# Kernel tuning notes

Hardware: AMD Instinct MI355X
Metric: run time of the kernel (lower is better)

## Reference

```python
import jax, jax.numpy as jnp
import numpy as np

B, K, DIN, D, NH, HD, FF = 16384, 64, 49, 16, 2, 8, 32
EPS = 1e-5


def _ln(x, g, b):
    m = jnp.mean(x, axis=-1, keepdims=True)
    v = jnp.mean((x - m) ** 2, axis=-1, keepdims=True)
    return (x - m) / jnp.sqrt(v + EPS) * g + b


def setup_inputs() -> dict:
    key = jax.random.key(0)
    ks = jax.random.split(key, 20)
    s = 0.05
    return {
        "x": jax.random.normal(ks[0], (B, K, DIN), dtype=jnp.float32),
        # torch Linear layout: weight is [out, in]
        "proj_w": jax.random.normal(ks[1], (D, DIN), dtype=jnp.float32) * s,
        "proj_b": jax.random.normal(ks[2], (D,), dtype=jnp.float32) * s,
        "pos": jax.random.normal(ks[3], (1, K, D), dtype=jnp.float32) * s,
        "in_proj_w": jax.random.normal(ks[4], (3 * D, D), dtype=jnp.float32) * s,
        "in_proj_b": jax.random.normal(ks[5], (3 * D,), dtype=jnp.float32) * s,
        "out_w": jax.random.normal(ks[6], (D, D), dtype=jnp.float32) * s,
        "out_b": jax.random.normal(ks[7], (D,), dtype=jnp.float32) * s,
        "ln1_g": jnp.ones((D,), dtype=jnp.float32),
        "ln1_b": jnp.zeros((D,), dtype=jnp.float32),
        "lin1_w": jax.random.normal(ks[8], (FF, D), dtype=jnp.float32) * s,
        "lin1_b": jax.random.normal(ks[9], (FF,), dtype=jnp.float32) * s,
        "lin2_w": jax.random.normal(ks[10], (D, FF), dtype=jnp.float32) * s,
        "lin2_b": jax.random.normal(ks[11], (D,), dtype=jnp.float32) * s,
        "ln2_g": jnp.ones((D,), dtype=jnp.float32),
        "ln2_b": jnp.zeros((D,), dtype=jnp.float32),
        "head_w": jax.random.normal(ks[12], (1, D), dtype=jnp.float32) * s,
        "head_b": jax.random.normal(ks[13], (1,), dtype=jnp.float32) * s,
    }


def reference(x, proj_w, proj_b, pos, in_proj_w, in_proj_b, out_w, out_b,
              ln1_g, ln1_b, lin1_w, lin1_b, lin2_w, lin2_b, ln2_g, ln2_b,
              head_w, head_b):
    # input projection + learned positional embedding
    h = jnp.einsum("bki,di->bkd", x, proj_w) + proj_b + pos  # [B,K,D]

    # --- self-attention (torch MultiheadAttention, post-norm encoder layer) ---
    qkv = jnp.einsum("bkd,ed->bke", h, in_proj_w) + in_proj_b  # [B,K,3D]
    q, k, v = jnp.split(qkv, 3, axis=-1)
    q = q.reshape(B, K, NH, HD)
    k = k.reshape(B, K, NH, HD)
    v = v.reshape(B, K, NH, HD)
    scores = jnp.einsum("bqhd,bkhd->bhqk", q, k) / jnp.sqrt(jnp.float32(HD))
    attn = jax.nn.softmax(scores, axis=-1)
    ctx = jnp.einsum("bhqk,bkhd->bqhd", attn, v).reshape(B, K, D)
    attn_out = jnp.einsum("bkd,od->bko", ctx, out_w) + out_b
    h = _ln(h + attn_out, ln1_g, ln1_b)

    # --- FFN (relu), post-norm ---
    ff = jnp.einsum("bkd,fd->bkf", h, lin1_w) + lin1_b
    ff = jax.nn.relu(ff)
    ff = jnp.einsum("bkf,df->bkd", ff, lin2_w) + lin2_b
    h = _ln(h + ff, ln2_g, ln2_b)

    # mean pool over sequence, then scalar head
    pooled = h.mean(axis=1)  # [B,D]
    out = jnp.einsum("bd,od->bo", pooled, head_w) + head_b
    return out.squeeze(-1)  # [B]
```

## Files before the change

### kernel.cpp

```cpp
#include <hip/hip_runtime.h>


#define XR   0
#define XRS  72
#define HR   4608
#define HRS  40
#define KR   7168
#define KRS  40
#define VTB  9728
#define VTS  72
#define RED  10880
#define SMTOT 10888

#define WS_HB   2304
#define WS_EP   3328

typedef __bf16 v8bf __attribute__((ext_vector_type(8)));
typedef float  v4f  __attribute__((ext_vector_type(4)));

#define LDS_ORDER() __asm__ volatile("" ::: "memory")

static __device__ __forceinline__ short f2bs(float f) {
    __bf16 h = (__bf16)f;
    return __builtin_bit_cast(short, h);
}
#define MFMA(a,b,c) __builtin_amdgcn_mfma_f32_16x16x32_bf16((a),(b),(c),0,0,0)

__global__ __launch_bounds__(64)
void tx_prep(const float* __restrict__ proj_w, const float* __restrict__ proj_b,
             const float* __restrict__ pos,
             const float* __restrict__ in_proj_w, const float* __restrict__ in_proj_b,
             const float* __restrict__ out_w, const float* __restrict__ out_b,
             const float* __restrict__ ln1_g, const float* __restrict__ ln1_b,
             const float* __restrict__ lin1_w, const float* __restrict__ lin1_b,
             const float* __restrict__ lin2_w, const float* __restrict__ lin2_b,
             const float* __restrict__ ln2_g, const float* __restrict__ ln2_b,
             const float* __restrict__ head_w, float* __restrict__ ws)
{
    const int lane = threadIdx.x, g = lane >> 4, c = lane & 15;
    v8bf* wf = (v8bf*)ws;
    v8bf F;
    #pragma unroll
    for (int j = 0; j < 8; ++j) F[j] = (__bf16)proj_w[c*49 + g*8 + j];
    wf[0*64 + lane] = F;
    #pragma unroll
    for (int j = 0; j < 8; ++j) { int k = 32 + g*8 + j; F[j] = (k < 49) ? (__bf16)proj_w[c*49 + k] : (__bf16)0.f; }
    wf[1*64 + lane] = F;
    #pragma unroll
    for (int nt = 0; nt < 3; ++nt) {
        #pragma unroll
        for (int j = 0; j < 8; ++j) { int k = g*8 + j; F[j] = (k < 16) ? (__bf16)in_proj_w[(nt*16 + c)*16 + k] : (__bf16)0.f; }
        wf[(2 + nt)*64 + lane] = F;
    }
    #pragma unroll
    for (int j = 0; j < 8; ++j) { int k = g*8 + j; F[j] = (k < 16) ? (__bf16)out_w[c*16 + k] : (__bf16)0.f; }
    wf[5*64 + lane] = F;
    #pragma unroll
    for (int nt = 0; nt < 2; ++nt) {
        #pragma unroll
        for (int j = 0; j < 8; ++j) { int k = g*8 + j; F[j] = (k < 16) ? (__bf16)lin1_w[(nt*16 + c)*16 + k] : (__bf16)0.f; }
        wf[(6 + nt)*64 + lane] = F;
    }
    #pragma unroll
    for (int j = 0; j < 8; ++j) F[j] = (__bf16)lin2_w[c*32 + g*8 + j];
    wf[8*64 + lane] = F;

    float* hb = ws + WS_HB;
    #pragma unroll
    for (int ww = 0; ww < 4; ++ww)
        #pragma unroll
        for (int r = 0; r < 4; ++r)
            hb[ww*256 + r*64 + lane] = proj_b[c] + pos[(ww*16 + g*4 + r)*16 + c];

    if (lane < 16) {
        float* ep = ws + WS_EP + lane*16;
        ep[0]  = in_proj_b[lane];
        ep[1]  = in_proj_b[16 + lane];
        ep[2]  = in_proj_b[32 + lane];
        ep[3]  = out_b[lane];
        ep[4]  = ln1_g[lane];
        ep[5]  = ln1_b[lane];
        ep[6]  = lin1_b[lane];
        ep[7]  = lin1_b[16 + lane];
        ep[8]  = lin2_b[lane];
        ep[9]  = ln2_g[lane];
        ep[10] = ln2_b[lane];
        ep[11] = head_w[lane];
        ep[12] = 0.f; ep[13] = 0.f; ep[14] = 0.f; ep[15] = 0.f;
    }
}

__global__ __launch_bounds__(256, 7)
void tx_main(const float* __restrict__ x, const float* __restrict__ ws,
             const float* __restrict__ head_b, float* __restrict__ out)
{
    __shared__ __align__(16) short sm[SMTOT];
    const int tid   = threadIdx.x;
    const int w     = tid >> 6;
    const int lane  = tid & 63;
    const int g     = lane >> 4;
    const int c     = lane & 15;
    const int b     = blockIdx.x;
    const int myrow = w*16 + c;
    const int tok0  = w*16 + g*4;
    const int sw    = (c >> 2) & 3;
    const v8bf* wf  = (const v8bf*)ws;
    const float4* ep4 = (const float4*)(ws + WS_EP);

    v8bf zfrag;
    #pragma unroll
    for (int j = 0; j < 8; ++j) zfrag[j] = (__bf16)0.f;

    const float4* xb4 = (const float4*)(x + (size_t)b * 3136);
    #pragma unroll
    for (int i = 0; i < 3; ++i) {
        int idx = tid + i*256;
        float4 v = xb4[idx];
        float vv[4] = {v.x, v.y, v.z, v.w};
        int flat = idx*4;
        #pragma unroll
        for (int e = 0; e < 4; ++e) {
            int f = flat + e, row = f / 49, col = f - row*49;
            int cs = (((col >> 3) ^ ((row >> 2) & 3)) << 3) | (col & 7);
            sm[XR + row*XRS + cs] = f2bs(vv[e]);
        }
    }
    if (tid < 16) {
        int idx = 768 + tid;
        float4 v = xb4[idx];
        float vv[4] = {v.x, v.y, v.z, v.w};
        int flat = idx*4;
        #pragma unroll
        for (int e = 0; e < 4; ++e) {
            int f = flat + e, row = f / 49, col = f - row*49;
            int cs = (((col >> 3) ^ ((row >> 2) & 3)) << 3) | (col & 7);
            sm[XR + row*XRS + cs] = f2bs(vv[e]);
        }
    }
    #pragma unroll
    for (int j = 0; j < 4; ++j) {
        int col = 49 + g*4 + j;
        if (col < 64) {
            int cs = (((col >> 3) ^ sw) << 3) | (col & 7);
            sm[XR + myrow*XRS + cs] = 0;
        }
    }
    *(unsigned long long*)&sm[HR + myrow*HRS + 16 + g*4] = 0ull;
    __syncthreads();

    v4f hC;
    {
        v8bf Bp0 = wf[0*64 + lane], Bp1 = wf[1*64 + lane];
        v8bf a0 = *(const v8bf*)&sm[XR + myrow*XRS + ((g ^ sw) << 3)];
        v8bf a1 = *(const v8bf*)&sm[XR + myrow*XRS + 32 + ((g ^ sw) << 3)];
        v4f z = {0.f, 0.f, 0.f, 0.f};
        hC = MFMA(a0, Bp0, z);
        hC = MFMA(a1, Bp1, hC);
        const float* hb = ws + WS_HB;
        #pragma unroll
        for (int r = 0; r < 4; ++r) hC[r] += hb[w*256 + r*64 + lane];
        #pragma unroll
        for (int r = 0; r < 4; ++r) sm[HR + (tok0 + r)*HRS + c] = f2bs(hC[r]);
    }
    LDS_ORDER();

    {
        v8bf Bq0 = wf[2*64 + lane], Bq1 = wf[3*64 + lane], Bq2 = wf[4*64 + lane];
        v8bf a = *(const v8bf*)&sm[HR + myrow*HRS + g*8];
        v4f z = {0.f, 0.f, 0.f, 0.f};
        v4f qC = MFMA(a, Bq0, z);
        v4f kC = MFMA(a, Bq1, z);
        v4f vC = MFMA(a, Bq2, z);
        float4 e0 = ep4[c*4];
        #pragma unroll
        for (int r = 0; r < 4; ++r) {
            int tok = tok0 + r;
            sm[HR + tok*HRS + c]   = f2bs(qC[r] + e0.x);
            sm[KR + tok*KRS + c]   = f2bs(kC[r] + e0.y);
            sm[VTB + c*VTS + tok]  = f2bs(vC[r] + e0.z);
        }
    }
    __syncthreads();

    v4f ctxC0, ctxC1;
    {
        v8bf aq = *(const v8bf*)&sm[HR + myrow*HRS + g*8];
        const float SC = 0.510069729f;
        #pragma unroll
        for (int hh = 0; hh < 2; ++hh) {
            v4f sC[4];
            #pragma unroll
            for (int tj = 0; tj < 4; ++tj) {
                v8bf bk = zfrag;
                if (g == hh) bk = *(const v8bf*)&sm[KR + (tj*16 + c)*KRS + g*8];
                v4f z = {0.f, 0.f, 0.f, 0.f};
                sC[tj] = MFMA(aq, bk, z);
            }
            #pragma unroll
            for (int tj = 0; tj < 4; ++tj) {
                int cl = ((((tj*2) + (c >> 3)) ^ g) << 3) | (c & 7);
                #pragma unroll
                for (int r = 0; r < 4; ++r)
                    sm[XR + (tok0 + r)*XRS + cl] = f2bs(exp2f(sC[tj][r] * SC));
            }
            v8bf bv0 = zfrag, bv1 = zfrag;
            bool act  = (hh == 0) ? (c < 8) : (c >= 8);
            int  onec = (hh == 0) ? 8 : 7;
            if (act) {
                bv0 = *(const v8bf*)&sm[VTB + c*VTS + g*8];
                bv1 = *(const v8bf*)&sm[VTB + c*VTS + 32 + g*8];
            } else if (c == onec) {
                #pragma unroll
                for (int j = 0; j < 8; ++j) { bv0[j] = (__bf16)1.f; bv1[j] = (__bf16)1.f; }
            }
            LDS_ORDER();
            v4f acc = {0.f, 0.f, 0.f, 0.f};
            acc = MFMA(*(const v8bf*)&sm[XR + myrow*XRS + ((g ^ sw) << 3)],      bv0, acc);
            acc = MFMA(*(const v8bf*)&sm[XR + myrow*XRS + 32 + ((g ^ sw) << 3)], bv1, acc);
            if (hh) ctxC1 = acc; else ctxC0 = acc;
            LDS_ORDER();
        }
    }

    {
        int src0 = (lane & 48) | 8;
        int src1 = (lane & 48) | 7;
        #pragma unroll
        for (int r = 0; r < 4; ++r) {
            float l0 = __shfl(ctxC0[r], src0, 64);
            float l1 = __shfl(ctxC1[r], src1, 64);
            float val = (c < 8) ? (ctxC0[r] / l0) : (ctxC1[r] / l1);
            sm[HR + (tok0 + r)*HRS + c] = f2bs(val);
        }
    }
    LDS_ORDER();

    v4f hln;
    {
        v8bf Bo = wf[5*64 + lane];
        v8bf a = *(const v8bf*)&sm[HR + myrow*HRS + g*8];
        v4f z = {0.f, 0.f, 0.f, 0.f};
        v4f oC = MFMA(a, Bo, z);
        float4 e0 = ep4[c*4];
        float4 e1 = ep4[c*4 + 1];
        v4f hn;
        #pragma unroll
        for (int r = 0; r < 4; ++r) hn[r] = hC[r] + oC[r] + e0.w;
        v4f s = hn;
        #pragma unroll
        for (int m = 1; m < 16; m <<= 1)
            #pragma unroll
            for (int r = 0; r < 4; ++r) s[r] += __shfl_xor(s[r], m, 64);
        v4f t, vs;
        #pragma unroll
        for (int r = 0; r < 4; ++r) { t[r] = hn[r] - s[r]*0.0625f; vs[r] = t[r]*t[r]; }
        #pragma unroll
        for (int m = 1; m < 16; m <<= 1)
            #pragma unroll
            for (int r = 0; r < 4; ++r) vs[r] += __shfl_xor(vs[r], m, 64);
        #pragma unroll
        for (int r = 0; r < 4; ++r) {
            float is = rsqrtf(vs[r]*0.0625f + 1e-5f);
            hln[r] = t[r]*is*e1.x + e1.y;
            sm[HR + (tok0 + r)*HRS + c] = f2bs(hln[r]);
        }
    }
    LDS_ORDER();

    v4f o2;
    {
        v8bf Bl10 = wf[6*64 + lane], Bl11 = wf[7*64 + lane], Bl2 = wf[8*64 + lane];
        v8bf a = *(const v8bf*)&sm[HR + myrow*HRS + g*8];
        v4f z = {0.f, 0.f, 0.f, 0.f};
        v4f f0 = MFMA(a, Bl10, z);
        v4f f1 = MFMA(a, Bl11, z);
        float4 e1 = ep4[c*4 + 1];
        #pragma unroll
        for (int r = 0; r < 4; ++r) {
            int tok = tok0 + r;
            sm[HR + tok*HRS + c]      = f2bs(fmaxf(f0[r] + e1.z, 0.f));
            sm[HR + tok*HRS + 16 + c] = f2bs(fmaxf(f1[r] + e1.w, 0.f));
        }
        LDS_ORDER();
        v8bf a2 = *(const v8bf*)&sm[HR + myrow*HRS + g*8];
        o2 = MFMA(a2, Bl2, z);
    }

    float part = 0.f;
    {
        float4 e2 = ep4[c*4 + 2];
        v4f hn;
        #pragma unroll
        for (int r = 0; r < 4; ++r) hn[r] = hln[r] + o2[r] + e2.x;
        v4f s = hn;
        #pragma unroll
        for (int m = 1; m < 16; m <<= 1)
            #pragma unroll
            for (int r = 0; r < 4; ++r) s[r] += __shfl_xor(s[r], m, 64);
        v4f t, vs;
        #pragma unroll
        for (int r = 0; r < 4; ++r) { t[r] = hn[r] - s[r]*0.0625f; vs[r] = t[r]*t[r]; }
        #pragma unroll
        for (int m = 1; m < 16; m <<= 1)
            #pragma unroll
            for (int r = 0; r < 4; ++r) vs[r] += __shfl_xor(vs[r], m, 64);
        #pragma unroll
        for (int r = 0; r < 4; ++r) {
            float is = rsqrtf(vs[r]*0.0625f + 1e-5f);
            float h3 = t[r]*is*e2.y + e2.z;
            part = fmaf(h3, e2.w, part);
        }
    }
    #pragma unroll
    for (int m = 1; m < 64; m <<= 1) part += __shfl_xor(part, m, 64);
    float* fred = (float*)&sm[RED];
    if (lane == 0) fred[w] = part;
    __syncthreads();
    if (tid == 0)
        out[b] = (fred[0] + fred[1] + fred[2] + fred[3]) * (1.f/64.f) + head_b[0];
}

extern "C" void kernel_launch(void* const* d_in, const int* in_sizes, int n_in,
                              void* d_out, int out_size, void* d_ws, size_t ws_size,
                              hipStream_t stream) {
    const float* x         = (const float*)d_in[0];
    const float* proj_w    = (const float*)d_in[1];
    const float* proj_b    = (const float*)d_in[2];
    const float* pos       = (const float*)d_in[3];
    const float* in_proj_w = (const float*)d_in[4];
    const float* in_proj_b = (const float*)d_in[5];
    const float* out_w     = (const float*)d_in[6];
    const float* out_b     = (const float*)d_in[7];
    const float* ln1_g     = (const float*)d_in[8];
    const float* ln1_b     = (const float*)d_in[9];
    const float* lin1_w    = (const float*)d_in[10];
    const float* lin1_b    = (const float*)d_in[11];
    const float* lin2_w    = (const float*)d_in[12];
    const float* lin2_b    = (const float*)d_in[13];
    const float* ln2_g     = (const float*)d_in[14];
    const float* ln2_b     = (const float*)d_in[15];
    const float* head_w    = (const float*)d_in[16];
    const float* head_b    = (const float*)d_in[17];
    float* ws = (float*)d_ws;

    tx_prep<<<1, 64, 0, stream>>>(proj_w, proj_b, pos, in_proj_w, in_proj_b,
                                  out_w, out_b, ln1_g, ln1_b, lin1_w, lin1_b,
                                  lin2_w, lin2_b, ln2_g, ln2_b, head_w, ws);
    tx_main<<<16384, 256, 0, stream>>>(x, ws, head_b, (float*)d_out);
}
```

Before: 368.9 us.

## Stage raw fp32 input in LDS, fold softmax scale into K, use swizzle reductions

The input tile is now copied straight into shared memory as fp32 float4s, replacing the per-element divide, swizzle and bf16 convert scatter. Conversion to bf16 happens when each wave builds its MFMA A fragments. The softmax scale is folded into the K projection and its bias, so the raw exp2 intrinsic can be applied to scores directly. Cross-lane shuffles in the layernorm and pooling reductions become ds_swizzle operations, and division and rsqrt become the hardware rcp and rsq intrinsics. This costs an extra block barrier after the projection, strided unaligned fp32 LDS reads for the A fragments, and slightly lower-precision math intrinsics.

```diff
diff --git a/kernel.cpp b/kernel.cpp
--- a/kernel.cpp
+++ b/kernel.cpp
@@ -1,15 +1,16 @@
 #include <hip/hip_runtime.h>
 
 
-#define XR   0
-#define XRS  72
-#define HR   4608
-#define HRS  40
-#define KR   7168
-#define KRS  40
-#define VTB  9728
-#define VTS  72
-#define RED  10880
+#define SCALE 0.510069729f
+
+#define KRS   40
+#define VTB   2560
+#define VTS   72
+#define PRB   3712
+#define PRS   72
+#define HRB   8320
+#define HRS   40
+#define RED   10880
 #define SMTOT 10888
 
 #define WS_HB   2304
@@ -25,6 +26,22 @@
     return __builtin_bit_cast(short, h);
 }
 #define MFMA(a,b,c) __builtin_amdgcn_mfma_f32_16x16x32_bf16((a),(b),(c),0,0,0)
+
+template<int IMM> static __device__ __forceinline__ float swz(float x) {
+    return __builtin_bit_cast(float,
+        __builtin_amdgcn_ds_swizzle(__builtin_bit_cast(int, x), IMM));
+}
+
+static __device__ __forceinline__ void red16(v4f& v) {
+    #pragma unroll
+    for (int r = 0; r < 4; ++r) v[r] += swz<0x041F>(v[r]);
+    #pragma unroll
+    for (int r = 0; r < 4; ++r) v[r] += swz<0x081F>(v[r]);
+    #pragma unroll
+    for (int r = 0; r < 4; ++r) v[r] += swz<0x101F>(v[r]);
+    #pragma unroll
+    for (int r = 0; r < 4; ++r) v[r] += swz<0x201F>(v[r]);
+}
 
 __global__ __launch_bounds__(64)
 void tx_prep(const float* __restrict__ proj_w, const float* __restrict__ proj_b,
@@ -75,7 +92,7 @@
     if (lane < 16) {
         float* ep = ws + WS_EP + lane*16;
         ep[0]  = in_proj_b[lane];
-        ep[1]  = in_proj_b[16 + lane];
+        ep[1]  = in_proj_b[16 + lane] * SCALE;
         ep[2]  = in_proj_b[32 + lane];
         ep[3]  = out_b[lane];
         ep[4]  = ln1_g[lane];
@@ -103,105 +120,81 @@
     const int b     = blockIdx.x;
     const int myrow = w*16 + c;
     const int tok0  = w*16 + g*4;
-    const int sw    = (c >> 2) & 3;
     const v8bf* wf  = (const v8bf*)ws;
     const float4* ep4 = (const float4*)(ws + WS_EP);
+    float* smf = (float*)sm;
 
     v8bf zfrag;
     #pragma unroll
     for (int j = 0; j < 8; ++j) zfrag[j] = (__bf16)0.f;
+    const v4f zacc = {0.f, 0.f, 0.f, 0.f};
 
     const float4* xb4 = (const float4*)(x + (size_t)b * 3136);
-    #pragma unroll
-    for (int i = 0; i < 3; ++i) {
-        int idx = tid + i*256;
-        float4 v = xb4[idx];
-        float vv[4] = {v.x, v.y, v.z, v.w};
-        int flat = idx*4;
-        #pragma unroll
-        for (int e = 0; e < 4; ++e) {
-            int f = flat + e, row = f / 49, col = f - row*49;
-            int cs = (((col >> 3) ^ ((row >> 2) & 3)) << 3) | (col & 7);
-            sm[XR + row*XRS + cs] = f2bs(vv[e]);
-        }
-    }
-    if (tid < 16) {
-        int idx = 768 + tid;
-        float4 v = xb4[idx];
-        float vv[4] = {v.x, v.y, v.z, v.w};
-        int flat = idx*4;
-        #pragma unroll
-        for (int e = 0; e < 4; ++e) {
-            int f = flat + e, row = f / 49, col = f - row*49;
-            int cs = (((col >> 3) ^ ((row >> 2) & 3)) << 3) | (col & 7);
-            sm[XR + row*XRS + cs] = f2bs(vv[e]);
-        }
-    }
-    #pragma unroll
-    for (int j = 0; j < 4; ++j) {
-        int col = 49 + g*4 + j;
-        if (col < 64) {
-            int cs = (((col >> 3) ^ sw) << 3) | (col & 7);
-            sm[XR + myrow*XRS + cs] = 0;
-        }
-    }
-    *(unsigned long long*)&sm[HR + myrow*HRS + 16 + g*4] = 0ull;
+    float4* sf4 = (float4*)smf;
+    #pragma unroll
+    for (int i = 0; i < 3; ++i) sf4[tid + i*256] = xb4[tid + i*256];
+    if (tid < 16)      sf4[768 + tid] = xb4[768 + tid];
+    else if (tid < 32) smf[3136 + tid - 16] = 0.f;
+    *(unsigned long long*)&sm[HRB + myrow*HRS + 16 + g*4] = 0ull;
     __syncthreads();
 
     v4f hC;
     {
+        const float* xr = smf + myrow*49 + g*8;
+        v8bf a0, a1;
+        #pragma unroll
+        for (int j = 0; j < 8; ++j) a0[j] = (__bf16)xr[j];
+        #pragma unroll
+        for (int j = 0; j < 8; ++j) a1[j] = (__bf16)xr[32 + j];
         v8bf Bp0 = wf[0*64 + lane], Bp1 = wf[1*64 + lane];
-        v8bf a0 = *(const v8bf*)&sm[XR + myrow*XRS + ((g ^ sw) << 3)];
-        v8bf a1 = *(const v8bf*)&sm[XR + myrow*XRS + 32 + ((g ^ sw) << 3)];
-        v4f z = {0.f, 0.f, 0.f, 0.f};
-        hC = MFMA(a0, Bp0, z);
+        hC = MFMA(a0, Bp0, zacc);
         hC = MFMA(a1, Bp1, hC);
         const float* hb = ws + WS_HB;
         #pragma unroll
         for (int r = 0; r < 4; ++r) hC[r] += hb[w*256 + r*64 + lane];
         #pragma unroll
-        for (int r = 0; r < 4; ++r) sm[HR + (tok0 + r)*HRS + c] = f2bs(hC[r]);
-    }
-    LDS_ORDER();
+        for (int r = 0; r < 4; ++r) sm[HRB + (tok0 + r)*HRS + c] = f2bs(hC[r]);
+    }
+    __syncthreads();
 
     {
         v8bf Bq0 = wf[2*64 + lane], Bq1 = wf[3*64 + lane], Bq2 = wf[4*64 + lane];
-        v8bf a = *(const v8bf*)&sm[HR + myrow*HRS + g*8];
-        v4f z = {0.f, 0.f, 0.f, 0.f};
-        v4f qC = MFMA(a, Bq0, z);
-        v4f kC = MFMA(a, Bq1, z);
-        v4f vC = MFMA(a, Bq2, z);
+        v8bf a = *(const v8bf*)&sm[HRB + myrow*HRS + g*8];
+        v4f qC = MFMA(a, Bq0, zacc);
+        v4f kC = MFMA(a, Bq1, zacc);
+        v4f vC = MFMA(a, Bq2, zacc);
         float4 e0 = ep4[c*4];
         #pragma unroll
         for (int r = 0; r < 4; ++r) {
             int tok = tok0 + r;
-            sm[HR + tok*HRS + c]   = f2bs(qC[r] + e0.x);
-            sm[KR + tok*KRS + c]   = f2bs(kC[r] + e0.y);
-            sm[VTB + c*VTS + tok]  = f2bs(vC[r] + e0.z);
+            sm[HRB + tok*HRS + c] = f2bs(qC[r] + e0.x);
+            sm[tok*KRS + c]       = f2bs(fmaf(kC[r], SCALE, e0.y));
+            sm[VTB + c*VTS + tok] = f2bs(vC[r] + e0.z);
         }
     }
     __syncthreads();
 
     v4f ctxC0, ctxC1;
     {
-        v8bf aq = *(const v8bf*)&sm[HR + myrow*HRS + g*8];
-        const float SC = 0.510069729f;
+        v8bf aq = *(const v8bf*)&sm[HRB + myrow*HRS + g*8];
+        const int ch  = c >> 3;
+        const int pwb = PRB + tok0*PRS + (c & 7);
+        const int prd = PRB + myrow*PRS + ((g ^ ((myrow >> 2) & 3)) << 3);
         #pragma unroll
         for (int hh = 0; hh < 2; ++hh) {
             v4f sC[4];
             #pragma unroll
             for (int tj = 0; tj < 4; ++tj) {
                 v8bf bk = zfrag;
-                if (g == hh) bk = *(const v8bf*)&sm[KR + (tj*16 + c)*KRS + g*8];
-                v4f z = {0.f, 0.f, 0.f, 0.f};
-                sC[tj] = MFMA(aq, bk, z);
+                if (g == hh) bk = *(const v8bf*)&sm[(tj*16 + c)*KRS + g*8];
+                sC[tj] = MFMA(aq, bk, zacc);
             }
             #pragma unroll
             for (int tj = 0; tj < 4; ++tj) {
-                int cl = ((((tj*2) + (c >> 3)) ^ g) << 3) | (c & 7);
+                int po = pwb + (((tj*2 + ch) ^ g) << 3);
                 #pragma unroll
                 for (int r = 0; r < 4; ++r)
-                    sm[XR + (tok0 + r)*XRS + cl] = f2bs(exp2f(sC[tj][r] * SC));
+                    sm[po + r*PRS] = f2bs(__builtin_amdgcn_exp2f(sC[tj][r]));
             }
             v8bf bv0 = zfrag, bv1 = zfrag;
             bool act  = (hh == 0) ? (c < 8) : (c >= 8);
@@ -214,23 +207,22 @@
                 for (int j = 0; j < 8; ++j) { bv0[j] = (__bf16)1.f; bv1[j] = (__bf16)1.f; }
             }
             LDS_ORDER();
-            v4f acc = {0.f, 0.f, 0.f, 0.f};
-            acc = MFMA(*(const v8bf*)&sm[XR + myrow*XRS + ((g ^ sw) << 3)],      bv0, acc);
-            acc = MFMA(*(const v8bf*)&sm[XR + myrow*XRS + 32 + ((g ^ sw) << 3)], bv1, acc);
+            v4f acc = zacc;
+            acc = MFMA(*(const v8bf*)&sm[prd],      bv0, acc);
+            acc = MFMA(*(const v8bf*)&sm[prd + 32], bv1, acc);
             if (hh) ctxC1 = acc; else ctxC0 = acc;
             LDS_ORDER();
         }
     }
 
     {
-        int src0 = (lane & 48) | 8;
-        int src1 = (lane & 48) | 7;
-        #pragma unroll
-        for (int r = 0; r < 4; ++r) {
-            float l0 = __shfl(ctxC0[r], src0, 64);
-            float l1 = __shfl(ctxC1[r], src1, 64);
-            float val = (c < 8) ? (ctxC0[r] / l0) : (ctxC1[r] / l1);
-            sm[HR + (tok0 + r)*HRS + c] = f2bs(val);
+        #pragma unroll
+        for (int r = 0; r < 4; ++r) {
+            float l0 = swz<0x110>(ctxC0[r]);
+            float l1 = swz<0x0F0>(ctxC1[r]);
+            float num = (c < 8) ? ctxC0[r] : ctxC1[r];
+            float den = (c < 8) ? l0 : l1;
+            sm[HRB + (tok0 + r)*HRS + c] = f2bs(num * __builtin_amdgcn_rcpf(den));
         }
     }
     LDS_ORDER();
@@ -238,31 +230,24 @@
     v4f hln;
     {
         v8bf Bo = wf[5*64 + lane];
-        v8bf a = *(const v8bf*)&sm[HR + myrow*HRS + g*8];
-        v4f z = {0.f, 0.f, 0.f, 0.f};
-        v4f oC = MFMA(a, Bo, z);
+        v8bf a = *(const v8bf*)&sm[HRB + myrow*HRS + g*8];
+        v4f oC = MFMA(a, Bo, zacc);
         float4 e0 = ep4[c*4];
         float4 e1 = ep4[c*4 + 1];
         v4f hn;
         #pragma unroll
         for (int r = 0; r < 4; ++r) hn[r] = hC[r] + oC[r] + e0.w;
         v4f s = hn;
-        #pragma unroll
-        for (int m = 1; m < 16; m <<= 1)
-            #pragma unroll
-            for (int r = 0; r < 4; ++r) s[r] += __shfl_xor(s[r], m, 64);
+        red16(s);
         v4f t, vs;
         #pragma unroll
         for (int r = 0; r < 4; ++r) { t[r] = hn[r] - s[r]*0.0625f; vs[r] = t[r]*t[r]; }
-        #pragma unroll
-        for (int m = 1; m < 16; m <<= 1)
-            #pragma unroll
-            for (int r = 0; r < 4; ++r) vs[r] += __shfl_xor(vs[r], m, 64);
-        #pragma unroll
-        for (int r = 0; r < 4; ++r) {
-            float is = rsqrtf(vs[r]*0.0625f + 1e-5f);
+        red16(vs);
+        #pragma unroll
+        for (int r = 0; r < 4; ++r) {
+            float is = __builtin_amdgcn_rsqf(fmaf(vs[r], 0.0625f, 1e-5f));
             hln[r] = t[r]*is*e1.x + e1.y;
-            sm[HR + (tok0 + r)*HRS + c] = f2bs(hln[r]);
+            sm[HRB + (tok0 + r)*HRS + c] = f2bs(hln[r]);
         }
     }
     LDS_ORDER();
@@ -270,20 +255,19 @@
     v4f o2;
     {
         v8bf Bl10 = wf[6*64 + lane], Bl11 = wf[7*64 + lane], Bl2 = wf[8*64 + lane];
-        v8bf a = *(const v8bf*)&sm[HR + myrow*HRS + g*8];
-        v4f z = {0.f, 0.f, 0.f, 0.f};
-        v4f f0 = MFMA(a, Bl10, z);
-        v4f f1 = MFMA(a, Bl11, z);
+        v8bf a = *(const v8bf*)&sm[HRB + myrow*HRS + g*8];
+        v4f f0 = MFMA(a, Bl10, zacc);
+        v4f f1 = MFMA(a, Bl11, zacc);
         float4 e1 = ep4[c*4 + 1];
         #pragma unroll
         for (int r = 0; r < 4; ++r) {
             int tok = tok0 + r;
-            sm[HR + tok*HRS + c]      = f2bs(fmaxf(f0[r] + e1.z, 0.f));
-            sm[HR + tok*HRS + 16 + c] = f2bs(fmaxf(f1[r] + e1.w, 0.f));
+            sm[HRB + tok*HRS + c]      = f2bs(fmaxf(f0[r] + e1.z, 0.f));
+            sm[HRB + tok*HRS + 16 + c] = f2bs(fmaxf(f1[r] + e1.w, 0.f));
         }
         LDS_ORDER();
-        v8bf a2 = *(const v8bf*)&sm[HR + myrow*HRS + g*8];
-        o2 = MFMA(a2, Bl2, z);
+        v8bf a2 = *(const v8bf*)&sm[HRB + myrow*HRS + g*8];
+        o2 = MFMA(a2, Bl2, zacc);
     }
 
     float part = 0.f;
@@ -293,26 +277,24 @@
         #pragma unroll
         for (int r = 0; r < 4; ++r) hn[r] = hln[r] + o2[r] + e2.x;
         v4f s = hn;
-        #pragma unroll
-        for (int m = 1; m < 16; m <<= 1)
-            #pragma unroll
-            for (int r = 0; r < 4; ++r) s[r] += __shfl_xor(s[r], m, 64);
+        red16(s);
         v4f t, vs;
         #pragma unroll
         for (int r = 0; r < 4; ++r) { t[r] = hn[r] - s[r]*0.0625f; vs[r] = t[r]*t[r]; }
-        #pragma unroll
-        for (int m = 1; m < 16; m <<= 1)
-            #pragma unroll
-            for (int r = 0; r < 4; ++r) vs[r] += __shfl_xor(vs[r], m, 64);
-        #pragma unroll
-        for (int r = 0; r < 4; ++r) {
-            float is = rsqrtf(vs[r]*0.0625f + 1e-5f);
+        red16(vs);
+        #pragma unroll
+        for (int r = 0; r < 4; ++r) {
+            float is = __builtin_amdgcn_rsqf(fmaf(vs[r], 0.0625f, 1e-5f));
             float h3 = t[r]*is*e2.y + e2.z;
             part = fmaf(h3, e2.w, part);
         }
     }
-    #pragma unroll
-    for (int m = 1; m < 64; m <<= 1) part += __shfl_xor(part, m, 64);
+    part += swz<0x041F>(part);
+    part += swz<0x081F>(part);
+    part += swz<0x101F>(part);
+    part += swz<0x201F>(part);
+    part += swz<0x401F>(part);
+    part += __shfl_xor(part, 32, 64);
     float* fred = (float*)&sm[RED];
     if (lane == 0) fred[w] = part;
     __syncthreads();
```

Result: faster. 336.0 us (-8.9%).
